# Kernel optimization log

Measured on AMD Instinct MI355X. Metric: run time of the kernel, lower is better.

The kernel has to match this reference:

```python
import jax, jax.numpy as jnp
import numpy as np

C = 8.0


def _linear_scan(alpha, xbeta):
    # h_t = alpha_t * h_{t-1} + xbeta_t, scan over time axis=1
    def combine(e1, e2):
        a1, b1 = e1
        a2, b2 = e2
        return a2 * a1, a2 * b1 + b2
    _, h = jax.lax.associative_scan(combine, (alpha, xbeta), axis=1)
    return h


def setup_inputs() -> dict:
    dim = 2048
    B, T = 4, 4096
    key = jax.random.key(0)
    k_x, k_wi, k_wg = jax.random.split(key, 3)
    std = dim ** -0.5
    x = jax.random.normal(k_x, (B, T, dim), dtype=jnp.float32)
    W_in = jax.random.normal(k_wi, (dim, dim), dtype=jnp.float32) * std
    b_in = jnp.zeros((dim,), dtype=jnp.float32)
    W_gate = jax.random.normal(k_wg, (dim, dim), dtype=jnp.float32) * std
    b_gate = jnp.zeros((dim,), dtype=jnp.float32)
    forget_lambda = jnp.linspace(-4.323, -9.0, dim, dtype=jnp.float32)
    return {"x": x, "W_in": W_in, "b_in": b_in, "W_gate": W_gate,
            "b_gate": b_gate, "forget_lambda": forget_lambda}


def reference(x, W_in, b_in, W_gate, b_gate, forget_lambda):
    # x: [B, T, D]
    input_gate = jnp.einsum('btd,ed->bte', x, W_in) + b_in
    recurrence_gate = jnp.einsum('btd,ed->bte', x, W_gate) + b_gate
    # alpha_t = exp(-C * softplus(lambda) * sigmoid(r_t))  per channel
    alpha = jnp.exp(-C * jax.nn.softplus(forget_lambda) * jax.nn.sigmoid(recurrence_gate))
    beta = jnp.sqrt(1.0 - alpha ** 2 + 1e-6)
    xbeta = beta * jax.nn.sigmoid(input_gate) * x
    return _linear_scan(alpha, xbeta)
```

## Files before the change

### kernel.cpp

```cpp
#include <hip/hip_runtime.h>

typedef unsigned short u16;
typedef unsigned int u32;

using bf16x8 = __attribute__((ext_vector_type(8))) __bf16;
using f32x4  = __attribute__((ext_vector_type(4))) float;
using u16x8  = __attribute__((ext_vector_type(8))) u16;

#define BB 4
#define TT 4096
#define DD 2048
#define MM 16384
#define KK 2048
#define NCHUNK 16
#define CLEN 256

__device__ __forceinline__ u16 f2bf(float f) {
    u32 u = __float_as_uint(f);
    u32 r = (u + 0x7FFFu + ((u >> 16) & 1u)) >> 16;
    return (u16)r;
}

__device__ __forceinline__ void gload_lds16(const void* g, void* l) {
    __builtin_amdgcn_global_load_lds(
        (const __attribute__((address_space(1))) void*)g,
        (__attribute__((address_space(3))) void*)l, 16, 0, 0);
}

__global__ __launch_bounds__(256) void cvt_kernel(const float* __restrict__ in,
                                                  u16* __restrict__ out, int n8) {
    int i = blockIdx.x * 256 + threadIdx.x;
    if (i >= n8) return;
    const f32x4* p = (const f32x4*)in + (size_t)i * 2;
    f32x4 a = p[0], b = p[1];
    u16x8 o;
    o[0] = f2bf(a[0]); o[1] = f2bf(a[1]); o[2] = f2bf(a[2]); o[3] = f2bf(a[3]);
    o[4] = f2bf(b[0]); o[5] = f2bf(b[1]); o[6] = f2bf(b[2]); o[7] = f2bf(b[3]);
    *((u16x8*)out + i) = o;
}

#define BMg 256
#define BNg 128
#define BKg 32
#define NT (KK / BKg)

#define MF(a_, b_, c_) __builtin_amdgcn_mfma_f32_16x16x32_bf16(a_, b_, c_, 0, 0, 0)

__global__ __launch_bounds__(512, 2) void gemm_lock2(
    const u16* __restrict__ xb, const u16* __restrict__ wib, const u16* __restrict__ wgb,
    const float* __restrict__ b_in, const float* __restrict__ b_gate,
    const float* __restrict__ lam, u32* __restrict__ pair)
{
    __shared__ u16 As[4][BMg * BKg];
    __shared__ u16 Bi[4][BNg * BKg];
    __shared__ u16 Bg[4][BNg * BKg];

    const int tid = threadIdx.x;
    const int bid = blockIdx.x;
    const int cpx = gridDim.x >> 3;
    const int swz = (bid & 7) * cpx + (bid >> 3);
    const int et = swz & 15;
    const int mt = swz >> 4;
    const size_t m0 = (size_t)mt * BMg;
    const size_t e0 = (size_t)et * BNg;

    const int lane = tid & 63;
    const int w = tid >> 6;
    const int wr = w >> 2;
    const int wc = w & 3;
    const int r15 = lane & 15;
    const int s4 = lane >> 4;

    const u16 *gA[2], *gBi, *gBg;
#pragma unroll
    for (int j = 0; j < 2; j++) {
        int L = j * 512 + tid;
        int row = L >> 2;
        int cs = (L & 3) ^ (row & 3) ^ ((row >> 2) & 3);
        gA[j] = xb + (m0 + row) * (size_t)KK + cs * 8;
    }
    {
        int row = tid >> 2;
        int cs = (tid & 3) ^ (row & 3) ^ ((row >> 2) & 3);
        gBi = wib + (e0 + row) * (size_t)KK + cs * 8;
        gBg = wgb + (e0 + row) * (size_t)KK + cs * 8;
    }

#define ST_A(t) do { int _s = (t) & 3; size_t _k = (size_t)(t) * BKg; \
        gload_lds16(gA[0] + _k, &As[_s][tid * 8]); \
        gload_lds16(gA[1] + _k, &As[_s][4096 + tid * 8]); } while (0)
#define ST_B(t) do { int _s = (t) & 3; size_t _k = (size_t)(t) * BKg; \
        gload_lds16(gBi + _k, &Bi[_s][tid * 8]); \
        gload_lds16(gBg + _k, &Bg[_s][tid * 8]); } while (0)

    const int csw = (s4 ^ (r15 & 3) ^ ((r15 >> 2) & 3)) << 3;
    int aR[8], bR[2];
#pragma unroll
    for (int mF = 0; mF < 8; mF++) aR[mF] = ((wr * 128 + mF * 16 + r15) << 5) + csw;
#pragma unroll
    for (int ni = 0; ni < 2; ni++) bR[ni] = ((wc * 32 + ni * 16 + r15) << 5) + csw;

    f32x4 accI[8][2], accG[8][2];
#pragma unroll
    for (int i = 0; i < 8; i++)
#pragma unroll
        for (int j = 0; j < 2; j++) {
            accI[i][j] = (f32x4){0.f, 0.f, 0.f, 0.f};
            accG[i][j] = (f32x4){0.f, 0.f, 0.f, 0.f};
        }

    bf16x8 aF[4], bv[4];

#define LGKM0() do { asm volatile("s_waitcnt lgkmcnt(0)" ::: "memory"); \
                     __builtin_amdgcn_sched_barrier(0); } while (0)
#define BURST(base) do { __builtin_amdgcn_s_setprio(1); \
        _Pragma("unroll") for (int m = 0; m < 4; m++) { \
            accI[m + (base)][0] = MF(aF[m], bv[0], accI[m + (base)][0]); \
            accI[m + (base)][1] = MF(aF[m], bv[1], accI[m + (base)][1]); \
            accG[m + (base)][0] = MF(aF[m], bv[2], accG[m + (base)][0]); \
            accG[m + (base)][1] = MF(aF[m], bv[3], accG[m + (base)][1]); } \
        __builtin_amdgcn_s_setprio(0); } while (0)

    ST_A(0); ST_B(0);
    ST_A(1); ST_B(1);
    asm volatile("s_waitcnt vmcnt(4)" ::: "memory");
    __builtin_amdgcn_s_barrier();

#pragma unroll 4
    for (int t = 0; t < NT; ++t) {
        const int s = t & 3;
#pragma unroll
        for (int m = 0; m < 4; m++) aF[m] = *(const bf16x8*)&As[s][aR[m]];
        bv[0] = *(const bf16x8*)&Bi[s][bR[0]];
        bv[1] = *(const bf16x8*)&Bi[s][bR[1]];
        bv[2] = *(const bf16x8*)&Bg[s][bR[0]];
        bv[3] = *(const bf16x8*)&Bg[s][bR[1]];
        if (t < NT - 2) ST_A(t + 2);
        __builtin_amdgcn_s_barrier();
        LGKM0();
        BURST(0);
        __builtin_amdgcn_s_barrier();
#pragma unroll
        for (int m = 0; m < 4; m++) aF[m] = *(const bf16x8*)&As[s][aR[m + 4]];
        if (t < NT - 2) ST_B(t + 2);
        __builtin_amdgcn_s_barrier();
        LGKM0();
        BURST(4);
        if (t == NT - 3)      asm volatile("s_waitcnt vmcnt(0)" ::: "memory");
        else if (t < NT - 3)  asm volatile("s_waitcnt vmcnt(4)" ::: "memory");
        __builtin_amdgcn_s_barrier();
    }

    float spl[2], biv[2], bgv[2];
    size_t ecol[2];
#pragma unroll
    for (int ni = 0; ni < 2; ni++) {
        size_t e = e0 + wc * 32 + ni * 16 + r15;
        ecol[ni] = e;
        spl[ni] = 8.0f * log1pf(__expf(lam[e]));
        biv[ni] = b_in[e];
        bgv[ni] = b_gate[e];
    }
    const int rbase = s4 * 4;
#pragma unroll
    for (int mi = 0; mi < 8; mi++) {
#pragma unroll
        for (int r = 0; r < 4; r++) {
            size_t m = m0 + wr * 128 + mi * 16 + rbase + r;
#pragma unroll
            for (int ni = 0; ni < 2; ni++) {
                size_t e = ecol[ni];
                float ig = accI[mi][ni][r] + biv[ni];
                float rg = accG[mi][ni][r] + bgv[ni];
                float sigr = 1.f / (1.f + __expf(-rg));
                float g = spl[ni] * sigr;
                float beta = sqrtf(1.f - __expf(-2.f * g) + 1e-6f);
                float xv = __uint_as_float((u32)xb[m * KK + e] << 16);
                float xbeta = beta * (1.f / (1.f + __expf(-ig))) * xv;
                u32 pk = (u32)f2bf(g) | (((u32)f2bf(xbeta)) << 16);
                pair[m * DD + e] = pk;
            }
        }
    }
#undef ST_A
#undef ST_B
#undef BURST
}

__global__ __launch_bounds__(256) void scanA(const u32* __restrict__ pair,
                                             float* __restrict__ aggG,
                                             float* __restrict__ aggB) {
    int gid = blockIdx.x * 256 + threadIdx.x;
    int e = gid & (DD - 1);
    int rest = gid >> 11;
    int b = rest & 3;
    int c = rest >> 2;
    const u32* p = pair + ((size_t)(b * TT + c * CLEN)) * DD + e;
    float gsum = 0.f, h = 0.f;
#pragma unroll 4
    for (int t = 0; t < CLEN; ++t) {
        u32 v = *p; p += DD;
        float gf = __uint_as_float(v << 16);
        float xbv = __uint_as_float(v & 0xFFFF0000u);
        gsum += gf;
        h = fmaf(__expf(-gf), h, xbv);
    }
    int idx = ((b * NCHUNK + c) << 11) | e;
    aggG[idx] = gsum;
    aggB[idx] = h;
}

__global__ __launch_bounds__(256) void scanB(const float* __restrict__ aggG,
                                             const float* __restrict__ aggB,
                                             float* __restrict__ carry) {
    int gid = blockIdx.x * 256 + threadIdx.x;
    int e = gid & (DD - 1);
    int b = gid >> 11;
    float h = 0.f;
#pragma unroll
    for (int c = 0; c < NCHUNK; ++c) {
        int idx = ((b * NCHUNK + c) << 11) | e;
        carry[idx] = h;
        h = fmaf(__expf(-aggG[idx]), h, aggB[idx]);
    }
}

__global__ __launch_bounds__(256) void scanC(const u32* __restrict__ pair,
                                             const float* __restrict__ carry,
                                             float* __restrict__ out) {
    int gid = blockIdx.x * 256 + threadIdx.x;
    int e = gid & (DD - 1);
    int rest = gid >> 11;
    int b = rest & 3;
    int c = rest >> 2;
    const u32* p = pair + ((size_t)(b * TT + c * CLEN)) * DD + e;
    float* o = out + ((size_t)(b * TT + c * CLEN)) * DD + e;
    float h = carry[((b * NCHUNK + c) << 11) | e];
#pragma unroll 4
    for (int t = 0; t < CLEN; ++t) {
        u32 v = *p; p += DD;
        float gf = __uint_as_float(v << 16);
        float xbv = __uint_as_float(v & 0xFFFF0000u);
        h = fmaf(__expf(-gf), h, xbv);
        *o = h; o += DD;
    }
}

extern "C" void kernel_launch(void* const* d_in, const int* in_sizes, int n_in,
                              void* d_out, int out_size, void* d_ws, size_t ws_size,
                              hipStream_t stream) {
    const float* x      = (const float*)d_in[0];
    const float* W_in   = (const float*)d_in[1];
    const float* b_in   = (const float*)d_in[2];
    const float* W_gate = (const float*)d_in[3];
    const float* b_gate = (const float*)d_in[4];
    const float* lam    = (const float*)d_in[5];
    float* out = (float*)d_out;

    char* ws = (char*)d_ws;
    u16* xb   = (u16*)(ws);
    u16* wib  = (u16*)(ws + 67108864);
    u16* wgb  = (u16*)(ws + 75497472);
    u32* pair = (u32*)(ws + 83886080);
    float* aggG  = (float*)(ws + 218103808);
    float* aggB  = (float*)(ws + 218628096);
    float* carry = (float*)(ws + 219152384);

    cvt_kernel<<<16384, 256, 0, stream>>>(x, xb, MM * KK / 8);
    cvt_kernel<<<2048, 256, 0, stream>>>(W_in, wib, DD * KK / 8);
    cvt_kernel<<<2048, 256, 0, stream>>>(W_gate, wgb, DD * KK / 8);
    gemm_lock2<<<(MM / BMg) * (DD / BNg), 512, 0, stream>>>(xb, wib, wgb, b_in, b_gate, lam, pair);
    scanA<<<BB * DD * NCHUNK / 256, 256, 0, stream>>>(pair, aggG, aggB);
    scanB<<<BB * DD / 256, 256, 0, stream>>>(aggG, aggB, carry);
    scanC<<<BB * DD * NCHUNK / 256, 256, 0, stream>>>(pair, carry, out);
}
```

Measured before the change: 472.8 us.

## Switch GEMM to 32x32x16 MFMA with 3-stage prefetch and finer scan chunks

Replaces the 16x16x32 MFMA tiling with 32x32x16 MFMA instructions, simplifying the LDS swizzle and fragment addressing. It deepens the global-to-LDS prefetch from two stages to three, with a peeled tail loop, to hide load latency. The scan is split into 32 chunks of 128 steps instead of 16 of 256 for more parallelism. Scan aggregates are placed in the region previously used for the bf16 weights, which risks aliasing if those buffers are still live.

```diff
diff --git a/kernel.cpp b/kernel.cpp
--- a/kernel.cpp
+++ b/kernel.cpp
@@ -5,6 +5,7 @@
 
 using bf16x8 = __attribute__((ext_vector_type(8))) __bf16;
 using f32x4  = __attribute__((ext_vector_type(4))) float;
+using f32x16 = __attribute__((ext_vector_type(16))) float;
 using u16x8  = __attribute__((ext_vector_type(8))) u16;
 
 #define BB 4
@@ -12,8 +13,8 @@
 #define DD 2048
 #define MM 16384
 #define KK 2048
-#define NCHUNK 16
-#define CLEN 256
+#define NCHUNK 32
+#define CLEN 128
 
 __device__ __forceinline__ u16 f2bf(float f) {
     u32 u = __float_as_uint(f);
@@ -44,9 +45,9 @@
 #define BKg 32
 #define NT (KK / BKg)
 
-#define MF(a_, b_, c_) __builtin_amdgcn_mfma_f32_16x16x32_bf16(a_, b_, c_, 0, 0, 0)
-
-__global__ __launch_bounds__(512, 2) void gemm_lock2(
+#define MF32(a_, b_, c_) __builtin_amdgcn_mfma_f32_32x32x16_bf16(a_, b_, c_, 0, 0, 0)
+
+__global__ __launch_bounds__(512, 2) void gemm_d32(
     const u16* __restrict__ xb, const u16* __restrict__ wib, const u16* __restrict__ wgb,
     const float* __restrict__ b_in, const float* __restrict__ b_gate,
     const float* __restrict__ lam, u32* __restrict__ pair)
@@ -68,22 +69,22 @@
     const int w = tid >> 6;
     const int wr = w >> 2;
     const int wc = w & 3;
-    const int r15 = lane & 15;
-    const int s4 = lane >> 4;
+    const int l31 = lane & 31;
+    const int lhi = lane >> 5;
 
     const u16 *gA[2], *gBi, *gBg;
 #pragma unroll
     for (int j = 0; j < 2; j++) {
         int L = j * 512 + tid;
         int row = L >> 2;
-        int cs = (L & 3) ^ (row & 3) ^ ((row >> 2) & 3);
-        gA[j] = xb + (m0 + row) * (size_t)KK + cs * 8;
+        int sc = (L & 3) ^ (row & 3);
+        gA[j] = xb + (m0 + row) * (size_t)KK + sc * 8;
     }
     {
         int row = tid >> 2;
-        int cs = (tid & 3) ^ (row & 3) ^ ((row >> 2) & 3);
-        gBi = wib + (e0 + row) * (size_t)KK + cs * 8;
-        gBg = wgb + (e0 + row) * (size_t)KK + cs * 8;
+        int sc = (tid & 3) ^ (row & 3);
+        gBi = wib + (e0 + row) * (size_t)KK + sc * 8;
+        gBg = wgb + (e0 + row) * (size_t)KK + sc * 8;
     }
 
 #define ST_A(t) do { int _s = (t) & 3; size_t _k = (size_t)(t) * BKg; \
@@ -93,87 +94,98 @@
         gload_lds16(gBi + _k, &Bi[_s][tid * 8]); \
         gload_lds16(gBg + _k, &Bg[_s][tid * 8]); } while (0)
 
-    const int csw = (s4 ^ (r15 & 3) ^ ((r15 >> 2) & 3)) << 3;
-    int aR[8], bR[2];
-#pragma unroll
-    for (int mF = 0; mF < 8; mF++) aR[mF] = ((wr * 128 + mF * 16 + r15) << 5) + csw;
-#pragma unroll
-    for (int ni = 0; ni < 2; ni++) bR[ni] = ((wc * 32 + ni * 16 + r15) << 5) + csw;
-
-    f32x4 accI[8][2], accG[8][2];
-#pragma unroll
-    for (int i = 0; i < 8; i++)
-#pragma unroll
-        for (int j = 0; j < 2; j++) {
-            accI[i][j] = (f32x4){0.f, 0.f, 0.f, 0.f};
-            accG[i][j] = (f32x4){0.f, 0.f, 0.f, 0.f};
-        }
+    int cswz[2];
+#pragma unroll
+    for (int kh = 0; kh < 2; kh++) cswz[kh] = (((kh * 2 + lhi) ^ (l31 & 3)) << 3);
+    int aR[4], bR;
+#pragma unroll
+    for (int mi = 0; mi < 4; mi++) aR[mi] = (wr * 128 + mi * 32 + l31) << 5;
+    bR = (wc * 32 + l31) << 5;
+
+    f32x16 acc[4][2];
+#pragma unroll
+    for (int mi = 0; mi < 4; mi++)
+#pragma unroll
+        for (int g = 0; g < 2; g++)
+#pragma unroll
+            for (int r = 0; r < 16; r++) acc[mi][g][r] = 0.f;
 
     bf16x8 aF[4], bv[4];
 
 #define LGKM0() do { asm volatile("s_waitcnt lgkmcnt(0)" ::: "memory"); \
                      __builtin_amdgcn_sched_barrier(0); } while (0)
-#define BURST(base) do { __builtin_amdgcn_s_setprio(1); \
-        _Pragma("unroll") for (int m = 0; m < 4; m++) { \
-            accI[m + (base)][0] = MF(aF[m], bv[0], accI[m + (base)][0]); \
-            accI[m + (base)][1] = MF(aF[m], bv[1], accI[m + (base)][1]); \
-            accG[m + (base)][0] = MF(aF[m], bv[2], accG[m + (base)][0]); \
-            accG[m + (base)][1] = MF(aF[m], bv[3], accG[m + (base)][1]); } \
+#define BURST(khsel) do { __builtin_amdgcn_s_setprio(1); \
+        _Pragma("unroll") for (int mi = 0; mi < 4; mi++) { \
+            acc[mi][0] = MF32(aF[mi], bv[0 + (khsel)], acc[mi][0]); \
+            acc[mi][1] = MF32(aF[mi], bv[2 + (khsel)], acc[mi][1]); } \
         __builtin_amdgcn_s_setprio(0); } while (0)
 
     ST_A(0); ST_B(0);
     ST_A(1); ST_B(1);
-    asm volatile("s_waitcnt vmcnt(4)" ::: "memory");
+    ST_A(2); ST_B(2);
+    asm volatile("s_waitcnt vmcnt(8)" ::: "memory");
     __builtin_amdgcn_s_barrier();
 
 #pragma unroll 4
-    for (int t = 0; t < NT; ++t) {
+    for (int t = 0; t < NT - 3; ++t) {
         const int s = t & 3;
 #pragma unroll
-        for (int m = 0; m < 4; m++) aF[m] = *(const bf16x8*)&As[s][aR[m]];
-        bv[0] = *(const bf16x8*)&Bi[s][bR[0]];
-        bv[1] = *(const bf16x8*)&Bi[s][bR[1]];
-        bv[2] = *(const bf16x8*)&Bg[s][bR[0]];
-        bv[3] = *(const bf16x8*)&Bg[s][bR[1]];
-        if (t < NT - 2) ST_A(t + 2);
+        for (int mi = 0; mi < 4; mi++) aF[mi] = *(const bf16x8*)&As[s][aR[mi] + cswz[0]];
+        bv[0] = *(const bf16x8*)&Bi[s][bR + cswz[0]];
+        bv[1] = *(const bf16x8*)&Bi[s][bR + cswz[1]];
+        bv[2] = *(const bf16x8*)&Bg[s][bR + cswz[0]];
+        bv[3] = *(const bf16x8*)&Bg[s][bR + cswz[1]];
+        ST_A(t + 3);
         __builtin_amdgcn_s_barrier();
         LGKM0();
         BURST(0);
         __builtin_amdgcn_s_barrier();
 #pragma unroll
-        for (int m = 0; m < 4; m++) aF[m] = *(const bf16x8*)&As[s][aR[m + 4]];
-        if (t < NT - 2) ST_B(t + 2);
-        __builtin_amdgcn_s_barrier();
-        LGKM0();
-        BURST(4);
-        if (t == NT - 3)      asm volatile("s_waitcnt vmcnt(0)" ::: "memory");
-        else if (t < NT - 3)  asm volatile("s_waitcnt vmcnt(4)" ::: "memory");
-        __builtin_amdgcn_s_barrier();
-    }
-
-    float spl[2], biv[2], bgv[2];
-    size_t ecol[2];
-#pragma unroll
-    for (int ni = 0; ni < 2; ni++) {
-        size_t e = e0 + wc * 32 + ni * 16 + r15;
-        ecol[ni] = e;
-        spl[ni] = 8.0f * log1pf(__expf(lam[e]));
-        biv[ni] = b_in[e];
-        bgv[ni] = b_gate[e];
-    }
-    const int rbase = s4 * 4;
-#pragma unroll
-    for (int mi = 0; mi < 8; mi++) {
-#pragma unroll
-        for (int r = 0; r < 4; r++) {
-            size_t m = m0 + wr * 128 + mi * 16 + rbase + r;
-#pragma unroll
-            for (int ni = 0; ni < 2; ni++) {
-                size_t e = ecol[ni];
-                float ig = accI[mi][ni][r] + biv[ni];
-                float rg = accG[mi][ni][r] + bgv[ni];
+        for (int mi = 0; mi < 4; mi++) aF[mi] = *(const bf16x8*)&As[s][aR[mi] + cswz[1]];
+        ST_B(t + 3);
+        __builtin_amdgcn_s_barrier();
+        LGKM0();
+        BURST(1);
+        asm volatile("s_waitcnt vmcnt(8)" ::: "memory");
+        __builtin_amdgcn_s_barrier();
+    }
+#pragma unroll 1
+    for (int t = NT - 3; t < NT; ++t) {
+        const int s = t & 3;
+#pragma unroll
+        for (int mi = 0; mi < 4; mi++) aF[mi] = *(const bf16x8*)&As[s][aR[mi] + cswz[0]];
+        bv[0] = *(const bf16x8*)&Bi[s][bR + cswz[0]];
+        bv[1] = *(const bf16x8*)&Bi[s][bR + cswz[1]];
+        bv[2] = *(const bf16x8*)&Bg[s][bR + cswz[0]];
+        bv[3] = *(const bf16x8*)&Bg[s][bR + cswz[1]];
+        __builtin_amdgcn_s_barrier();
+        LGKM0();
+        BURST(0);
+        __builtin_amdgcn_s_barrier();
+#pragma unroll
+        for (int mi = 0; mi < 4; mi++) aF[mi] = *(const bf16x8*)&As[s][aR[mi] + cswz[1]];
+        __builtin_amdgcn_s_barrier();
+        LGKM0();
+        BURST(1);
+        if (t == NT - 3)      asm volatile("s_waitcnt vmcnt(4)" ::: "memory");
+        else if (t == NT - 2) asm volatile("s_waitcnt vmcnt(0)" ::: "memory");
+        __builtin_amdgcn_s_barrier();
+    }
+
+    {
+        size_t e = e0 + wc * 32 + l31;
+        float spl = 8.0f * log1pf(__expf(lam[e]));
+        float biv = b_in[e];
+        float bgv = b_gate[e];
+#pragma unroll
+        for (int mi = 0; mi < 4; mi++) {
+#pragma unroll
+            for (int r = 0; r < 16; r++) {
+                size_t m = m0 + wr * 128 + mi * 32 + (r & 3) + 8 * (r >> 2) + 4 * lhi;
+                float ig = acc[mi][0][r] + biv;
+                float rg = acc[mi][1][r] + bgv;
                 float sigr = 1.f / (1.f + __expf(-rg));
-                float g = spl[ni] * sigr;
+                float g = spl * sigr;
                 float beta = sqrtf(1.f - __expf(-2.f * g) + 1e-6f);
                 float xv = __uint_as_float((u32)xb[m * KK + e] << 16);
                 float xbeta = beta * (1.f / (1.f + __expf(-ig))) * xv;
@@ -262,14 +274,14 @@
     u16* wib  = (u16*)(ws + 67108864);
     u16* wgb  = (u16*)(ws + 75497472);
     u32* pair = (u32*)(ws + 83886080);
-    float* aggG  = (float*)(ws + 218103808);
-    float* aggB  = (float*)(ws + 218628096);
-    float* carry = (float*)(ws + 219152384);
+    float* aggG  = (float*)(ws + 67108864);
+    float* aggB  = (float*)(ws + 68157440);
+    float* carry = (float*)(ws + 69206016);
 
     cvt_kernel<<<16384, 256, 0, stream>>>(x, xb, MM * KK / 8);
     cvt_kernel<<<2048, 256, 0, stream>>>(W_in, wib, DD * KK / 8);
     cvt_kernel<<<2048, 256, 0, stream>>>(W_gate, wgb, DD * KK / 8);
-    gemm_lock2<<<(MM / BMg) * (DD / BNg), 512, 0, stream>>>(xb, wib, wgb, b_in, b_gate, lam, pair);
+    gemm_d32<<<(MM / BMg) * (DD / BNg), 512, 0, stream>>>(xb, wib, wgb, b_in, b_gate, lam, pair);
     scanA<<<BB * DD * NCHUNK / 256, 256, 0, stream>>>(pair, aggG, aggB);
     scanB<<<BB * DD / 256, 256, 0, stream>>>(aggG, aggB, carry);
     scanC<<<BB * DD * NCHUNK / 256, 256, 0, stream>>>(pair, carry, out);
```

New measurement: 489.1 us. 1.03x slower.
